# Kernel tuning notes

Measured on AMD Instinct MI355X. Metric: run time of the kernel, lower is better.

Reference implementation:

```python
import jax, jax.numpy as jnp
import numpy as np

N_SAMPLES = 32768
N_EVENTS = 64
STEP_SIZE = 256  # indices * STEP_SIZE gives the time offset of each event
BATCH = 16


def setup_inputs() -> dict:
    key = jax.random.key(0)
    k1, k2 = jax.random.split(key)
    x = jax.random.normal(k1, (BATCH, N_EVENTS, N_SAMPLES), dtype=jnp.float32)
    # indices in [0, n_samples/step_size] so time + n_samples <= 2*n_samples
    indices = jax.random.randint(k2, (BATCH, N_EVENTS), 0, N_SAMPLES // STEP_SIZE, dtype=jnp.int64)
    return {"x": x, "indices": indices}


def reference(x, indices):
    # x: [B, E, S] event signals; indices: [B, E] int offsets (in units of step_size)
    B, E, S = x.shape
    times = indices * STEP_SIZE  # [B, E]
    # per-sample target positions in the double-length buffer: [B, E, S]
    pos = times[:, :, None].astype(jnp.int32) + jnp.arange(S, dtype=jnp.int32)[None, None, :]

    def scatter_one(vals, p):
        # vals: [E, S], p: [E, S] -> scatter-add into length-2S buffer
        return jnp.zeros(2 * S, vals.dtype).at[p.reshape(-1)].add(vals.reshape(-1))

    out = jax.vmap(scatter_one)(x, pos)  # [B, 2S]
    # truncate to n_samples, add channel dim -> [B, 1, S]
    return out[:, None, :S]
```

## Files before the change

### kernel.cpp

```cpp
#include <hip/hip_runtime.h>

constexpr int B = 16;
constexpr int E = 64;
constexpr int S = 32768;
constexpr int STEP = 256;
constexpr int SAMPLES_PER_BLOCK = 1024;
constexpr int GRP = 16;

__global__ __launch_bounds__(256)
void sparse_audio_gather(const float* __restrict__ x,
                         const int* __restrict__ idx,
                         float* __restrict__ out) {
    const int b  = blockIdx.y;
    const int s0 = blockIdx.x * SAMPLES_PER_BLOCK + threadIdx.x * 4;

    __shared__ int t_lds[E];
    if (threadIdx.x < E) {
        t_lds[threadIdx.x] = idx[b * E + threadIdx.x] * STEP;
    }
    __syncthreads();

    const float* xb = x + (size_t)b * E * S;

    float4 acc = make_float4(0.f, 0.f, 0.f, 0.f);

    for (int e0 = 0; e0 < E; e0 += GRP) {
        float4 v[GRP];
        float  m[GRP];
        #pragma unroll
        for (int j = 0; j < GRP; ++j) {
            const int off  = s0 - t_lds[e0 + j];
            const int offc = off < 0 ? 0 : off;
            m[j] = off < 0 ? 0.0f : 1.0f;
            v[j] = *reinterpret_cast<const float4*>(
                       xb + (size_t)(e0 + j) * S + offc);
        }
        #pragma unroll
        for (int j = 0; j < GRP; ++j) {
            acc.x += m[j] * v[j].x;
            acc.y += m[j] * v[j].y;
            acc.z += m[j] * v[j].z;
            acc.w += m[j] * v[j].w;
        }
    }

    *reinterpret_cast<float4*>(out + (size_t)b * S + s0) = acc;
}

extern "C" void kernel_launch(void* const* d_in, const int* in_sizes, int n_in,
                              void* d_out, int out_size, void* d_ws, size_t ws_size,
                              hipStream_t stream) {
    const float* x   = (const float*)d_in[0];
    const int*   idx = (const int*)d_in[1];
    float*       out = (float*)d_out;

    dim3 grid(S / SAMPLES_PER_BLOCK, B);
    dim3 block(256);
    sparse_audio_gather<<<grid, block, 0, stream>>>(x, idx, out);
}
```

Measured before the change: 175.8 us.

## Split event dimension across blocks and reduce partial sums in second kernel

Adds a grid dimension that splits the 64 events into 8 groups, so each block gathers and sums only 8 events and writes a partial result to workspace. A second kernel then sums the 8 partials into the output. The aim is to raise the block count far above the original 512, improving occupancy and memory-level parallelism for this latency-bound gather. In exchange it adds a second launch, extra workspace traffic and a dependence on the workspace being at least 16 MB.

```diff
diff --git a/kernel.cpp b/kernel.cpp
--- a/kernel.cpp
+++ b/kernel.cpp
@@ -5,56 +5,80 @@
 constexpr int S = 32768;
 constexpr int STEP = 256;
 constexpr int SAMPLES_PER_BLOCK = 1024;
-constexpr int GRP = 16;
+constexpr int ESPLIT = 8;
+constexpr int EPB = E / ESPLIT;
 
 __global__ __launch_bounds__(256)
-void sparse_audio_gather(const float* __restrict__ x,
-                         const int* __restrict__ idx,
-                         float* __restrict__ out) {
+void gather_partial(const float* __restrict__ x,
+                    const int* __restrict__ idx,
+                    float* __restrict__ part) {
     const int b  = blockIdx.y;
+    const int ez = blockIdx.z;
     const int s0 = blockIdx.x * SAMPLES_PER_BLOCK + threadIdx.x * 4;
 
-    __shared__ int t_lds[E];
-    if (threadIdx.x < E) {
-        t_lds[threadIdx.x] = idx[b * E + threadIdx.x] * STEP;
+    __shared__ int t_lds[EPB];
+    if (threadIdx.x < EPB) {
+        t_lds[threadIdx.x] = idx[b * E + ez * EPB + threadIdx.x] * STEP;
     }
     __syncthreads();
 
-    const float* xb = x + (size_t)b * E * S;
+    const float* xb = x + ((size_t)b * E + (size_t)ez * EPB) * S;
+
+    float4 v[EPB];
+    float  m[EPB];
+    #pragma unroll
+    for (int j = 0; j < EPB; ++j) {
+        const int off  = s0 - t_lds[j];
+        const int offc = off < 0 ? 0 : off;
+        m[j] = off < 0 ? 0.0f : 1.0f;
+        v[j] = *reinterpret_cast<const float4*>(xb + (size_t)j * S + offc);
+    }
 
     float4 acc = make_float4(0.f, 0.f, 0.f, 0.f);
-
-    for (int e0 = 0; e0 < E; e0 += GRP) {
-        float4 v[GRP];
-        float  m[GRP];
-        #pragma unroll
-        for (int j = 0; j < GRP; ++j) {
-            const int off  = s0 - t_lds[e0 + j];
-            const int offc = off < 0 ? 0 : off;
-            m[j] = off < 0 ? 0.0f : 1.0f;
-            v[j] = *reinterpret_cast<const float4*>(
-                       xb + (size_t)(e0 + j) * S + offc);
-        }
-        #pragma unroll
-        for (int j = 0; j < GRP; ++j) {
-            acc.x += m[j] * v[j].x;
-            acc.y += m[j] * v[j].y;
-            acc.z += m[j] * v[j].z;
-            acc.w += m[j] * v[j].w;
-        }
+    #pragma unroll
+    for (int j = 0; j < EPB; ++j) {
+        acc.x += m[j] * v[j].x;
+        acc.y += m[j] * v[j].y;
+        acc.z += m[j] * v[j].z;
+        acc.w += m[j] * v[j].w;
     }
 
-    *reinterpret_cast<float4*>(out + (size_t)b * S + s0) = acc;
+    *reinterpret_cast<float4*>(part + ((size_t)ez * B + b) * S + s0) = acc;
+}
+
+__global__ __launch_bounds__(256)
+void reduce_partials(const float* __restrict__ part,
+                     float* __restrict__ out) {
+    const size_t i = ((size_t)blockIdx.x * 256 + threadIdx.x) * 4;
+
+    float4 v[ESPLIT];
+    #pragma unroll
+    for (int p = 0; p < ESPLIT; ++p) {
+        v[p] = *reinterpret_cast<const float4*>(part + (size_t)p * B * S + i);
+    }
+    float4 acc = make_float4(0.f, 0.f, 0.f, 0.f);
+    #pragma unroll
+    for (int p = 0; p < ESPLIT; ++p) {
+        acc.x += v[p].x;
+        acc.y += v[p].y;
+        acc.z += v[p].z;
+        acc.w += v[p].w;
+    }
+    *reinterpret_cast<float4*>(out + i) = acc;
 }
 
 extern "C" void kernel_launch(void* const* d_in, const int* in_sizes, int n_in,
                               void* d_out, int out_size, void* d_ws, size_t ws_size,
                               hipStream_t stream) {
-    const float* x   = (const float*)d_in[0];
-    const int*   idx = (const int*)d_in[1];
-    float*       out = (float*)d_out;
+    const float* x    = (const float*)d_in[0];
+    const int*   idx  = (const int*)d_in[1];
+    float*       out  = (float*)d_out;
+    float*       part = (float*)d_ws;
 
-    dim3 grid(S / SAMPLES_PER_BLOCK, B);
-    dim3 block(256);
-    sparse_audio_gather<<<grid, block, 0, stream>>>(x, idx, out);
+    dim3 grid1(S / SAMPLES_PER_BLOCK, B, ESPLIT);
+    gather_partial<<<grid1, dim3(256), 0, stream>>>(x, idx, part);
+
+    const int total = B * S;
+    dim3 grid2(total / (256 * 4));
+    reduce_partials<<<grid2, dim3(256), 0, stream>>>(part, out);
 }
```

Result: slower. 184.9 us (+5.2%).
